# Kernel optimization log

Hardware: AMD Instinct MI355X
Metric: run time of the kernel (lower is better)

Reference implementation:

```python
import jax, jax.numpy as jnp
import numpy as np

B, T, C = 4, 2048, 1024
H = 16
D = C // H  # head_dim = 64

def setup_inputs() -> dict:
    key = jax.random.key(0)
    ks = jax.random.split(key, 5)
    scale = 0.02
    x = jax.random.normal(ks[0], (B, T, C), dtype=jnp.float32)
    # weights stored [in, out] (transpose of torch Linear layout; same math)
    Wqkv = jax.random.normal(ks[1], (C, 3 * C), dtype=jnp.float32) * scale
    bqkv = jnp.zeros((3 * C,), dtype=jnp.float32)
    Wproj = jax.random.normal(ks[2], (C, C), dtype=jnp.float32) * scale
    bproj = jnp.zeros((C,), dtype=jnp.float32)
    return {"x": x, "Wqkv": Wqkv, "bqkv": bqkv, "Wproj": Wproj, "bproj": bproj}

def reference(x, Wqkv, bqkv, Wproj, bproj):
    Bx, Tx, Cx = x.shape
    qkv = x @ Wqkv + bqkv                      # [B,T,3C]
    q, k, v = jnp.split(qkv, 3, axis=2)
    # [B,T,C] -> [B,H,T,D]
    q = q.reshape(Bx, Tx, H, D).transpose(0, 2, 1, 3)
    k = k.reshape(Bx, Tx, H, D).transpose(0, 2, 1, 3)
    v = v.reshape(Bx, Tx, H, D).transpose(0, 2, 1, 3)
    att = jnp.einsum('bhqd,bhkd->bhqk', q, k) / jnp.sqrt(jnp.float32(D))
    causal = jnp.tril(jnp.ones((Tx, Tx), dtype=bool))
    att = jnp.where(causal, att, jnp.float32(-jnp.inf))
    att = jax.nn.softmax(att, axis=-1)
    y = jnp.einsum('bhqk,bhkd->bhqd', att, v)  # [B,H,T,D]
    y = y.transpose(0, 2, 1, 3).reshape(Bx, Tx, Cx)
    return y @ Wproj + bproj
```

## Files before the change

### kernel.cpp

```cpp
#include <hip/hip_runtime.h>
#include <math.h>

#define Bb 4
#define Tt 2048
#define Cc 1024
#define Hh 16
#define Dd 64
#define QSC 0.18033688011112042f

typedef unsigned short ushort_t;
typedef __attribute__((ext_vector_type(8))) short short8;
typedef __attribute__((ext_vector_type(4))) float floatx4;

typedef unsigned int __attribute__((address_space(1))) u32_as1;
typedef unsigned int __attribute__((address_space(3))) u32_as3;

__device__ __forceinline__ void gld_lds16(const void* g, const void* lds_uniform) {
    __builtin_amdgcn_global_load_lds(
        (const u32_as1*)(unsigned long long)g,
        (u32_as3*)(unsigned int)(unsigned long long)lds_uniform,
        16, 0, 0);
}

__device__ inline ushort_t f2bf(float x) {
    unsigned int u = __float_as_uint(x);
    return (ushort_t)((u + 0x7FFFu + ((u >> 16) & 1u)) >> 16);
}

__device__ __forceinline__ void bar() {
    asm volatile("" ::: "memory");
    __builtin_amdgcn_s_barrier();
    asm volatile("" ::: "memory");
}

__global__ __launch_bounds__(256) void convert_kernel(
    const float* __restrict__ in, ushort_t* __restrict__ out, int n4)
{
    int i = blockIdx.x * 256 + threadIdx.x;
    if (i < n4) {
        float4 v = *(const float4*)&in[i * 4];
        ushort_t o[4] = {f2bf(v.x), f2bf(v.y), f2bf(v.z), f2bf(v.w)};
        *(uint2*)&out[i * 4] = *(uint2*)o;
    }
}

__global__ __launch_bounds__(256) void transpose_kernel(
    const float* __restrict__ W, ushort_t* __restrict__ Wt, int K, int N)
{
    __shared__ ushort_t Ts[16][72];
    const int n0 = blockIdx.x * 64;
    const int k0 = blockIdx.y * 16;
    const int t = threadIdx.x;
#pragma unroll
    for (int i = 0; i < 4; i++) {
        int e = t + i * 256;
        int kl = e >> 6, nl = e & 63;
        Ts[kl][nl] = f2bf(W[(size_t)(k0 + kl) * N + n0 + nl]);
    }
    __syncthreads();
    {
        int nl = t >> 2, kl4 = (t & 3) * 4;
        ushort_t o[4] = {Ts[kl4][nl], Ts[kl4 + 1][nl], Ts[kl4 + 2][nl], Ts[kl4 + 3][nl]};
        *(uint2*)&Wt[(size_t)(n0 + nl) * K + k0 + kl4] = *(uint2*)o;
    }
}

template <bool OUT_BF16, bool SCALE_Q>
__global__ __launch_bounds__(512) void gemm128_kernel(
    const ushort_t* __restrict__ A, const ushort_t* __restrict__ Bt,
    const float* __restrict__ bias, void* __restrict__ Co,
    int M, int N, int K)
{
    __shared__ __align__(16) ushort_t Ls[49152];

    const int tid = threadIdx.x;
    const int lane = tid & 63;
    const int w = tid >> 6;
    const int wm = w >> 2, wn = w & 3;
    const int l = lane & 15, q = lane >> 4;
    const int NT = K >> 6;

    const int n0 = blockIdx.x * 256;
    const int m0 = blockIdx.y * 128;

    const int ln = lane ^ (((lane >> 5) & 1) << 1);
    const ushort_t* Ag = A  + (size_t)(m0 + w * 16 + (ln >> 2)) * K + (ln & 3) * 8;
    const ushort_t* Bg = Bt + (size_t)(n0 + w * 16 + (ln >> 2)) * K + (ln & 3) * 8;

    const int swz = l * 32 + ((q * 8) ^ (((l >> 3) & 1) << 4));

    floatx4 acc[2][4][2];
#pragma unroll
    for (int qn = 0; qn < 2; qn++)
#pragma unroll
        for (int mf = 0; mf < 4; mf++)
#pragma unroll
            for (int nf = 0; nf < 2; nf++)
                acc[qn][mf][nf] = (floatx4){0.f, 0.f, 0.f, 0.f};

    short8 af[4][2], bf0[2][2], bf1[2][2];

#define STAGE_A(SLOT, T) {                                                      \
    const ushort_t* _g = Ag + (size_t)(T) * 64;                                 \
    const ushort_t* _l = &Ls[(SLOT) * 24576 + w * 1024];                        \
    gld_lds16(_g, _l);                                                          \
    gld_lds16(_g + 32, _l + 512); }
#define STAGE_B(SLOT, H, T) {                                                   \
    const ushort_t* _g = Bg + (size_t)(H) * 128 * K + (size_t)(T) * 64;         \
    const ushort_t* _l = &Ls[(SLOT) * 24576 + (1 + (H)) * 8192 + w * 1024];     \
    gld_lds16(_g, _l);                                                          \
    gld_lds16(_g + 32, _l + 512); }

#define LDA(SLOT) {                                                             \
    _Pragma("unroll") for (int mf = 0; mf < 4; mf++)                            \
    _Pragma("unroll") for (int kc = 0; kc < 2; kc++)                            \
        af[mf][kc] = *(const short8*)&Ls[(SLOT) * 24576 +                       \
            ((wm * 4 + mf) * 2 + kc) * 512 + swz]; }

#define LDB(SLOT, QN, DST) {                                                    \
    _Pragma("unroll") for (int nf = 0; nf < 2; nf++)                            \
    _Pragma("unroll") for (int kc = 0; kc < 2; kc++)                            \
        DST[nf][kc] = *(const short8*)&Ls[(SLOT) * 24576 + (1 + (QN)) * 8192 +  \
            ((wn * 2 + nf) * 2 + kc) * 512 + swz]; }

#define MM(QN, BF) {                                                            \
    __builtin_amdgcn_s_setprio(1);                                              \
    _Pragma("unroll") for (int kc = 0; kc < 2; kc++)                            \
    _Pragma("unroll") for (int mf = 0; mf < 4; mf++)                            \
    _Pragma("unroll") for (int nf = 0; nf < 2; nf++)                            \
        acc[QN][mf][nf] = __builtin_amdgcn_mfma_f32_16x16x32_bf16(              \
            af[mf][kc], BF[nf][kc], acc[QN][mf][nf], 0, 0, 0);                  \
    __builtin_amdgcn_s_setprio(0); }

#define LGKM0() asm volatile("s_waitcnt lgkmcnt(0)" ::: "memory")

    STAGE_A(0, 0); STAGE_B(0, 0, 0); STAGE_B(0, 1, 0);
    if (NT > 1) {
        STAGE_A(1, 1); STAGE_B(1, 0, 1);
        asm volatile("s_waitcnt vmcnt(4)" ::: "memory");
    } else {
        asm volatile("s_waitcnt vmcnt(0)" ::: "memory");
    }
    bar();

    for (int g = 0; g < NT; ++g) {
        const int slot = g & 1;

        LDA(slot);
        LDB(slot, 0, bf0);
        if (g + 1 < NT) STAGE_B(slot ^ 1, 1, g + 1);
        bar();
        LGKM0();
        MM(0, bf0);
        bar();

        LDB(slot, 1, bf1);
        if (g + 2 < NT) { STAGE_A(slot, g + 2); STAGE_B(slot, 0, g + 2); }
        bar();
        LGKM0();
        MM(1, bf1);
        if (g + 1 < NT) {
            if (g + 2 < NT) asm volatile("s_waitcnt vmcnt(4)" ::: "memory");
            else            asm volatile("s_waitcnt vmcnt(0)" ::: "memory");
            bar();
        }
    }

#pragma unroll
    for (int qn = 0; qn < 2; qn++)
#pragma unroll
        for (int nf = 0; nf < 2; nf++) {
            const int col = n0 + qn * 128 + wn * 32 + nf * 16 + l;
            const float bi = bias[col];
            const float sc = (SCALE_Q && col < 1024) ? QSC : 1.0f;
#pragma unroll
            for (int mf = 0; mf < 4; mf++)
#pragma unroll
                for (int r = 0; r < 4; r++) {
                    const int row = m0 + wm * 64 + mf * 16 + q * 4 + r;
                    const float v = (acc[qn][mf][nf][r] + bi) * sc;
                    if (OUT_BF16)
                        ((ushort_t*)Co)[(size_t)row * N + col] = f2bf(v);
                    else
                        ((float*)Co)[(size_t)row * N + col] = v;
                }
        }
#undef STAGE_A
#undef STAGE_B
#undef LDA
#undef LDB
#undef MM
#undef LGKM0
}

__device__ __forceinline__ int ks_swz(int I) {
    return I ^ (((I >> 8) & 1) * 0x28) ^ (((I >> 9) & 1) * 0x10);
}
__device__ __forceinline__ int vt_idx(int row, int col) {
    return row * 80 + (col ^ ((((row >> 2) ^ (row >> 4)) & 3) << 3));
}
__device__ __forceinline__ int ps_idx(int row, int col) {
    return row * 80 + (col ^ (((row >> 2) & 3) << 3));
}

#define KS_SLOT 4096
#define VT_SLOT 6400

__global__ __launch_bounds__(256, 2) void attn_mfma_kernel(
    const ushort_t* __restrict__ qkv, ushort_t* __restrict__ yatt)
{
    __shared__ __align__(16) ushort_t Ks[2 * KS_SLOT];
    __shared__ __align__(16) ushort_t Vt[2 * VT_SLOT];
    __shared__ __align__(16) ushort_t Ps[4][2 * 1280];

    const int tid = threadIdx.x;
    const int lane = tid & 63;
    const int w = tid >> 6;
    const int quad = lane >> 4;
    const int l = lane & 15;

    const int bh = blockIdx.x;
    const int j = 15 - (int)blockIdx.y;
    const int q0 = j * 128;
    const int b = bh >> 4;
    const int h = bh & 15;
    const size_t base = (size_t)b * Tt * (3 * Cc);
    const int qoff = h * 64;
    const int koff = Cc + h * 64;
    const int voff = 2 * Cc + h * 64;

    for (int i = tid; i < 16 * 64; i += 256) {
        const int vi = vt_idx(64 + i / 64, i % 64);
        Vt[vi] = 0x3F80;
        Vt[VT_SLOT + vi] = 0x3F80;
    }

    short8 Qf[2][2];
#pragma unroll
    for (int mt = 0; mt < 2; mt++)
#pragma unroll
        for (int kc = 0; kc < 2; kc++)
            Qf[mt][kc] = *(const short8*)&qkv[base
                + (size_t)(q0 + mt * 64 + w * 16 + l) * (3 * Cc)
                + qoff + kc * 32 + quad * 8];

    floatx4 Oacc[2][4];
    floatx4 Lacc[2];
#pragma unroll
    for (int mt = 0; mt < 2; mt++) {
        Lacc[mt] = (floatx4){0.f, 0.f, 0.f, 0.f};
#pragma unroll
        for (int dt = 0; dt < 4; dt++)
            Oacc[mt][dt] = (floatx4){0.f, 0.f, 0.f, 0.f};
    }

    const int srow = tid >> 2;
    const int sd0 = (tid & 3) * 16;
    const int knt = srow >> 4, kl = srow & 15;
    const int kc_s = sd0 >> 5;
    const int qp0 = (sd0 & 31) >> 3;
    const int pcol = (srow & 15) * 4 + (srow >> 4);

    const int ntil = 2 * j + 2;

    const ushort_t* kp0 = &qkv[base + (size_t)srow * (3 * Cc) + koff + sd0];
    const ushort_t* vp0 = &qkv[base + (size_t)srow * (3 * Cc) + voff + sd0];

    const int ksw0 = ks_swz((knt * 2 + kc_s) * 512 + (qp0 * 16 + kl) * 8);
    const int ksw1 = ks_swz((knt * 2 + kc_s) * 512 + ((qp0 + 1) * 16 + kl) * 8);

    uint4 pk0 = *(const uint4*)kp0;
    uint4 pk1 = *(const uint4*)(kp0 + 8);
    uint4 pv0 = *(const uint4*)vp0;
    uint4 pv1 = *(const uint4*)(vp0 + 8);

#define WRITE_TILE(SLOT) {                                                      \
    *(uint4*)&Ks[(SLOT) * KS_SLOT + ksw0] = pk0;                                \
    *(uint4*)&Ks[(SLOT) * KS_SLOT + ksw1] = pk1;                                \
    ushort_t tv[16];                                                            \
    *(uint4*)&tv[0] = pv0;                                                      \
    *(uint4*)&tv[8] = pv1;                                                      \
    _Pragma("unroll") for (int t2 = 0; t2 < 16; t2++)                           \
        Vt[(SLOT) * VT_SLOT + vt_idx(sd0 + t2, pcol)] = tv[t2]; }

#define LOAD_TILE(KT) {                                                         \
    const size_t _off = (size_t)((KT) * 64) * (3 * Cc);                         \
    pk0 = *(const uint4*)(kp0 + _off);                                          \
    pk1 = *(const uint4*)(kp0 + _off + 8);                                      \
    pv0 = *(const uint4*)(vp0 + _off);                                          \
    pv1 = *(const uint4*)(vp0 + _off + 8); }

#define SOFTMAX(SV, MT) {                                                       \
    const int qminX = q0 + (MT) * 64 + (w << 4);                                \
    const bool needm = (kbase + 63 > qminX);                                    \
    _Pragma("unroll") for (int r = 0; r < 4; r++) {                             \
        const int qrow = qminX + quad * 4 + r;                                  \
        float e[4];                                                             \
        _Pragma("unroll") for (int nt = 0; nt < 4; nt++) {                      \
            float s2 = SV[nt][r];                                               \
            if (needm && (kbase + nt * 16 + l > qrow)) s2 = -INFINITY;          \
            e[nt] = __builtin_amdgcn_exp2f(s2);                                 \
        }                                                                       \
        unsigned int u0 = __builtin_amdgcn_perm(                                \
            __float_as_uint(e[1]), __float_as_uint(e[0]), 0x07060302u);         \
        unsigned int u1 = __builtin_amdgcn_perm(                                \
            __float_as_uint(e[3]), __float_as_uint(e[2]), 0x07060302u);         \
        uint2 pq; pq.x = u0; pq.y = u1;                                         \
        *(uint2*)&Ps[w][(MT) * 1280 + ps_idx(quad * 4 + r, l * 4)] = pq; } }

#define PVACC(MT) {                                                             \
    short8 Pa0 = *(const short8*)&Ps[w][(MT) * 1280 + ps_idx(l, quad * 8)];     \
    short8 Pa1 = *(const short8*)&Ps[w][(MT) * 1280 + ps_idx(l, 32 + quad * 8)];\
    __builtin_amdgcn_s_setprio(1);                                              \
    _Pragma("unroll") for (int dt = 0; dt < 4; dt++) {                          \
        Oacc[MT][dt] = __builtin_amdgcn_mfma_f32_16x16x32_bf16(                 \
            Pa0, Vf[dt][0], Oacc[MT][dt], 0, 0, 0);                             \
        Oacc[MT][dt] = __builtin_amdgcn_mfma_f32_16x16x32_bf16(                 \
            Pa1, Vf[dt][1], Oacc[MT][dt], 0, 0, 0);                             \
    }                                                                           \
    Lacc[MT] = __builtin_amdgcn_mfma_f32_16x16x32_bf16(                         \
        Pa0, Vf[4][0], Lacc[MT], 0, 0, 0);                                      \
    Lacc[MT] = __builtin_amdgcn_mfma_f32_16x16x32_bf16(                         \
        Pa1, Vf[4][1], Lacc[MT], 0, 0, 0);                                      \
    __builtin_amdgcn_s_setprio(0); }

    WRITE_TILE(0);
    if (ntil > 1) LOAD_TILE(1);
    __syncthreads();

    for (int kt = 0; kt < ntil; kt++) {
        const int kbase = kt * 64;
        const int slot = kt & 1;

        short8 Vf[5][2];
#pragma unroll
        for (int dt = 0; dt < 5; dt++)
#pragma unroll
            for (int kc = 0; kc < 2; kc++)
                Vf[dt][kc] = *(const short8*)&Vt[slot * VT_SLOT
                    + vt_idx(dt * 16 + l, kc * 32 + quad * 8)];

        if (kt + 1 < ntil) {
            WRITE_TILE(slot ^ 1);
            if (kt + 2 < ntil) LOAD_TILE(kt + 2);
        }

        const int qmin0 = q0 + (w << 4);
        const bool act0 = (kbase <= qmin0 + 15);

        floatx4 S1[4], S0[4];
#pragma unroll
        for (int nt = 0; nt < 4; nt++) S1[nt] = (floatx4){0.f, 0.f, 0.f, 0.f};
        __builtin_amdgcn_s_setprio(1);
        if (act0) {
#pragma unroll
            for (int nt = 0; nt < 4; nt++) S0[nt] = (floatx4){0.f, 0.f, 0.f, 0.f};
#pragma unroll
            for (int kc = 0; kc < 2; kc++)
#pragma unroll
                for (int nt = 0; nt < 4; nt++) {
                    short8 kf = *(const short8*)&Ks[slot * KS_SLOT
                        + ks_swz((nt * 2 + kc) * 512 + lane * 8)];
                    S1[nt] = __builtin_amdgcn_mfma_f32_16x16x32_bf16(
                        Qf[1][kc], kf, S1[nt], 0, 0, 0);
                    S0[nt] = __builtin_amdgcn_mfma_f32_16x16x32_bf16(
                        Qf[0][kc], kf, S0[nt], 0, 0, 0);
                }
        } else {
#pragma unroll
            for (int kc = 0; kc < 2; kc++)
#pragma unroll
                for (int nt = 0; nt < 4; nt++) {
                    short8 kf = *(const short8*)&Ks[slot * KS_SLOT
                        + ks_swz((nt * 2 + kc) * 512 + lane * 8)];
                    S1[nt] = __builtin_amdgcn_mfma_f32_16x16x32_bf16(
                        Qf[1][kc], kf, S1[nt], 0, 0, 0);
                }
        }
        __builtin_amdgcn_s_setprio(0);

        SOFTMAX(S1, 1);
        if (act0) SOFTMAX(S0, 0);
        asm volatile("" ::: "memory");

        PVACC(1);
        if (act0) PVACC(0);

        __syncthreads();
    }

#pragma unroll
    for (int mt = 0; mt < 2; mt++)
#pragma unroll
        for (int r = 0; r < 4; r++) {
            const float rl = 1.f / Lacc[mt][r];
            const int qrow = q0 + mt * 64 + (w << 4) + quad * 4 + r;
#pragma unroll
            for (int dt = 0; dt < 4; dt++)
                yatt[(size_t)(b * Tt + qrow) * Cc + h * 64 + dt * 16 + l] =
                    f2bf(Oacc[mt][dt][r] * rl);
        }
#undef WRITE_TILE
#undef LOAD_TILE
#undef SOFTMAX
#undef PVACC
}

extern "C" void kernel_launch(void* const* d_in, const int* in_sizes, int n_in,
                              void* d_out, int out_size, void* d_ws, size_t ws_size,
                              hipStream_t stream) {
    const float* x     = (const float*)d_in[0];
    const float* Wqkv  = (const float*)d_in[1];
    const float* bqkv  = (const float*)d_in[2];
    const float* Wproj = (const float*)d_in[3];
    const float* bproj = (const float*)d_in[4];
    float* out = (float*)d_out;

    ushort_t* qkvb   = (ushort_t*)d_ws;
    ushort_t* yattb  = qkvb + (size_t)8192 * 3072;
    ushort_t* xb     = yattb + (size_t)8192 * 1024;
    ushort_t* wqkvt  = xb + (size_t)8192 * 1024;
    ushort_t* wprojt = wqkvt + (size_t)3072 * 1024;

    convert_kernel<<<(8192 * 1024 / 4 + 255) / 256, 256, 0, stream>>>(x, xb, 8192 * 1024 / 4);
    transpose_kernel<<<dim3(3072 / 64, 1024 / 16), 256, 0, stream>>>(Wqkv, wqkvt, 1024, 3072);
    transpose_kernel<<<dim3(1024 / 64, 1024 / 16), 256, 0, stream>>>(Wproj, wprojt, 1024, 1024);

    gemm128_kernel<true, true><<<dim3(3072 / 256, 8192 / 128), 512, 0, stream>>>(
        xb, wqkvt, bqkv, qkvb, 8192, 3072, 1024);
    attn_mfma_kernel<<<dim3(64, 16), 256, 0, stream>>>(qkvb, yattb);
    gemm128_kernel<false, false><<<dim3(1024 / 256, 8192 / 128), 512, 0, stream>>>(
        yattb, wprojt, bproj, out, 8192, 1024, 1024);
}
```

Baseline: 256.8 us.

## Keep softmax probabilities in registers by transposing S MFMA operands

Swaps the operand order of the QK^T MFMA so each lane holds S values along the key dimension, which lets the exponentiated probabilities be packed directly into the A-operand of the PV MFMA without a round trip through shared memory. The V tile's key ordering is permuted (pcol) to match the new register layout. The row-sum is accumulated with explicit adds and cross-lane shuffles instead of an extra MFMA against a ones column, so the ones rows and the Ps LDS buffer are dropped. This removes LDS writes and reads plus two MFMAs per tile and cuts LDS footprint, at the cost of a few shuffles and more VALU adds.

Result: no change. 255.8 us (-0.4%).

```diff
diff --git a/kernel.cpp b/kernel.cpp
--- a/kernel.cpp
+++ b/kernel.cpp
@@ -199,19 +199,15 @@
 __device__ __forceinline__ int vt_idx(int row, int col) {
     return row * 80 + (col ^ ((((row >> 2) ^ (row >> 4)) & 3) << 3));
 }
-__device__ __forceinline__ int ps_idx(int row, int col) {
-    return row * 80 + (col ^ (((row >> 2) & 3) << 3));
-}
 
 #define KS_SLOT 4096
-#define VT_SLOT 6400
+#define VT_SLOT 5120
 
 __global__ __launch_bounds__(256, 2) void attn_mfma_kernel(
     const ushort_t* __restrict__ qkv, ushort_t* __restrict__ yatt)
 {
     __shared__ __align__(16) ushort_t Ks[2 * KS_SLOT];
     __shared__ __align__(16) ushort_t Vt[2 * VT_SLOT];
-    __shared__ __align__(16) ushort_t Ps[4][2 * 1280];
 
     const int tid = threadIdx.x;
     const int lane = tid & 63;
@@ -229,12 +225,6 @@
     const int koff = Cc + h * 64;
     const int voff = 2 * Cc + h * 64;
 
-    for (int i = tid; i < 16 * 64; i += 256) {
-        const int vi = vt_idx(64 + i / 64, i % 64);
-        Vt[vi] = 0x3F80;
-        Vt[VT_SLOT + vi] = 0x3F80;
-    }
-
     short8 Qf[2][2];
 #pragma unroll
     for (int mt = 0; mt < 2; mt++)
@@ -245,21 +235,20 @@
                 + qoff + kc * 32 + quad * 8];
 
     floatx4 Oacc[2][4];
-    floatx4 Lacc[2];
-#pragma unroll
-    for (int mt = 0; mt < 2; mt++) {
-        Lacc[mt] = (floatx4){0.f, 0.f, 0.f, 0.f};
+    float Lacc[2] = {0.f, 0.f};
+#pragma unroll
+    for (int mt = 0; mt < 2; mt++)
 #pragma unroll
         for (int dt = 0; dt < 4; dt++)
             Oacc[mt][dt] = (floatx4){0.f, 0.f, 0.f, 0.f};
-    }
 
     const int srow = tid >> 2;
     const int sd0 = (tid & 3) * 16;
     const int knt = srow >> 4, kl = srow & 15;
     const int kc_s = sd0 >> 5;
     const int qp0 = (sd0 & 31) >> 3;
-    const int pcol = (srow & 15) * 4 + (srow >> 4);
+    const int pcol = 32 * (srow >> 5) + 8 * ((srow >> 2) & 3)
+                   + 4 * ((srow >> 4) & 1) + (srow & 3);
 
     const int ntil = 2 * j + 2;
 
@@ -290,27 +279,32 @@
     pv0 = *(const uint4*)(vp0 + _off);                                          \
     pv1 = *(const uint4*)(vp0 + _off + 8); }
 
-#define SOFTMAX(SV, MT) {                                                       \
-    const int qminX = q0 + (MT) * 64 + (w << 4);                                \
-    const bool needm = (kbase + 63 > qminX);                                    \
-    _Pragma("unroll") for (int r = 0; r < 4; r++) {                             \
-        const int qrow = qminX + quad * 4 + r;                                  \
+#define SM_PV(SV, MT) {                                                         \
+    const int qrow = q0 + (MT) * 64 + (w << 4) + l;                             \
+    const bool needm = (kbase + 63 > q0 + (MT) * 64 + (w << 4));                \
+    float lsum = 0.f;                                                           \
+    unsigned int pw[8];                                                         \
+    _Pragma("unroll") for (int nt = 0; nt < 4; nt++) {                          \
         float e[4];                                                             \
-        _Pragma("unroll") for (int nt = 0; nt < 4; nt++) {                      \
+        _Pragma("unroll") for (int r = 0; r < 4; r++) {                         \
             float s2 = SV[nt][r];                                               \
-            if (needm && (kbase + nt * 16 + l > qrow)) s2 = -INFINITY;          \
-            e[nt] = __builtin_amdgcn_exp2f(s2);                                 \
+            if (needm && (kbase + nt * 16 + quad * 4 + r > qrow))               \
+                s2 = -INFINITY;                                                 \
+            e[r] = __builtin_amdgcn_exp2f(s2);                                  \
+            lsum += e[r];                                                       \
         }                                                                       \
-        unsigned int u0 = __builtin_amdgcn_perm(                                \
+        pw[nt * 2 + 0] = __builtin_amdgcn_perm(                                 \
             __float_as_uint(e[1]), __float_as_uint(e[0]), 0x07060302u);         \
-        unsigned int u1 = __builtin_amdgcn_perm(                                \
+        pw[nt * 2 + 1] = __builtin_amdgcn_perm(                                 \
             __float_as_uint(e[3]), __float_as_uint(e[2]), 0x07060302u);         \
-        uint2 pq; pq.x = u0; pq.y = u1;                                         \
-        *(uint2*)&Ps[w][(MT) * 1280 + ps_idx(quad * 4 + r, l * 4)] = pq; } }
-
-#define PVACC(MT) {                                                             \
-    short8 Pa0 = *(const short8*)&Ps[w][(MT) * 1280 + ps_idx(l, quad * 8)];     \
-    short8 Pa1 = *(const short8*)&Ps[w][(MT) * 1280 + ps_idx(l, 32 + quad * 8)];\
+    }                                                                           \
+    lsum += __shfl_xor(lsum, 16);                                               \
+    lsum += __shfl_xor(lsum, 32);                                               \
+    Lacc[MT] += lsum;                                                           \
+    uint4 _u0; _u0.x = pw[0]; _u0.y = pw[1]; _u0.z = pw[2]; _u0.w = pw[3];      \
+    uint4 _u1; _u1.x = pw[4]; _u1.y = pw[5]; _u1.z = pw[6]; _u1.w = pw[7];      \
+    short8 Pa0 = __builtin_bit_cast(short8, _u0);                               \
+    short8 Pa1 = __builtin_bit_cast(short8, _u1);                               \
     __builtin_amdgcn_s_setprio(1);                                              \
     _Pragma("unroll") for (int dt = 0; dt < 4; dt++) {                          \
         Oacc[MT][dt] = __builtin_amdgcn_mfma_f32_16x16x32_bf16(                 \
@@ -318,10 +312,6 @@
         Oacc[MT][dt] = __builtin_amdgcn_mfma_f32_16x16x32_bf16(                 \
             Pa1, Vf[dt][1], Oacc[MT][dt], 0, 0, 0);                             \
     }                                                                           \
-    Lacc[MT] = __builtin_amdgcn_mfma_f32_16x16x32_bf16(                         \
-        Pa0, Vf[4][0], Lacc[MT], 0, 0, 0);                                      \
-    Lacc[MT] = __builtin_amdgcn_mfma_f32_16x16x32_bf16(                         \
-        Pa1, Vf[4][1], Lacc[MT], 0, 0, 0);                                      \
     __builtin_amdgcn_s_setprio(0); }
 
     WRITE_TILE(0);
@@ -332,9 +322,9 @@
         const int kbase = kt * 64;
         const int slot = kt & 1;
 
-        short8 Vf[5][2];
-#pragma unroll
-        for (int dt = 0; dt < 5; dt++)
+        short8 Vf[4][2];
+#pragma unroll
+        for (int dt = 0; dt < 4; dt++)
 #pragma unroll
             for (int kc = 0; kc < 2; kc++)
                 Vf[dt][kc] = *(const short8*)&Vt[slot * VT_SLOT
@@ -362,9 +352,9 @@
                     short8 kf = *(const short8*)&Ks[slot * KS_SLOT
                         + ks_swz((nt * 2 + kc) * 512 + lane * 8)];
                     S1[nt] = __builtin_amdgcn_mfma_f32_16x16x32_bf16(
-                        Qf[1][kc], kf, S1[nt], 0, 0, 0);
+                        kf, Qf[1][kc], S1[nt], 0, 0, 0);
                     S0[nt] = __builtin_amdgcn_mfma_f32_16x16x32_bf16(
-                        Qf[0][kc], kf, S0[nt], 0, 0, 0);
+                        kf, Qf[0][kc], S0[nt], 0, 0, 0);
                 }
         } else {
 #pragma unroll
@@ -374,17 +364,13 @@
                     short8 kf = *(const short8*)&Ks[slot * KS_SLOT
                         + ks_swz((nt * 2 + kc) * 512 + lane * 8)];
                     S1[nt] = __builtin_amdgcn_mfma_f32_16x16x32_bf16(
-                        Qf[1][kc], kf, S1[nt], 0, 0, 0);
+                        kf, Qf[1][kc], S1[nt], 0, 0, 0);
                 }
         }
         __builtin_amdgcn_s_setprio(0);
 
-        SOFTMAX(S1, 1);
-        if (act0) SOFTMAX(S0, 0);
-        asm volatile("" ::: "memory");
-
-        PVACC(1);
-        if (act0) PVACC(0);
+        SM_PV(S1, 1);
+        if (act0) SM_PV(S0, 0);
 
         __syncthreads();
     }
@@ -393,7 +379,8 @@
     for (int mt = 0; mt < 2; mt++)
 #pragma unroll
         for (int r = 0; r < 4; r++) {
-            const float rl = 1.f / Lacc[mt][r];
+            const float Lr = __shfl(Lacc[mt], quad * 4 + r);
+            const float rl = 1.f / Lr;
             const int qrow = q0 + mt * 64 + (w << 4) + quad * 4 + r;
 #pragma unroll
             for (int dt = 0; dt < 4; dt++)
@@ -402,8 +389,7 @@
         }
 #undef WRITE_TILE
 #undef LOAD_TILE
-#undef SOFTMAX
-#undef PVACC
+#undef SM_PV
 }
 
 extern "C" void kernel_launch(void* const* d_in, const int* in_sizes, int n_in,
```
